# Optimization experiments

Measured on AMD Instinct MI355X. Metric: run time of the kernel, lower is better.

## Reference

```python
import jax, jax.numpy as jnp
import numpy as np

N = 50000        # nodes
E = 800000       # edges (avg degree 16)
C_IN = 64        # input_channels
H = 64           # hidden_channels
SLOPE = 0.01     # F.leaky_relu default negative_slope


def setup_inputs() -> dict:
    key = jax.random.key(0)
    ks = jax.random.split(key, 12)
    inp = {}
    inp["x"] = jax.random.normal(ks[0], (N, C_IN), dtype=jnp.float32)
    inp["edge_index"] = jax.random.randint(ks[1], (2, E), 0, N, dtype=jnp.int32)
    # SAGEConv params: lin_l (neighbors, with bias), lin_r (root, no bias)
    dims = [(C_IN, H), (H, H), (H, H)]
    for i, (ci, co) in enumerate(dims, start=1):
        s = 1.0 / np.sqrt(ci)
        inp[f"W_l{i}"] = jax.random.uniform(ks[2 * i], (ci, co), jnp.float32, -s, s)
        inp[f"b_l{i}"] = jnp.zeros((co,), jnp.float32)
        inp[f"W_r{i}"] = jax.random.uniform(ks[2 * i + 1], (ci, co), jnp.float32, -s, s)
    s = 1.0 / np.sqrt(H)
    inp["W_out"] = jax.random.uniform(ks[8], (H, 1), jnp.float32, -s, s)
    inp["b_out"] = jnp.zeros((1,), jnp.float32)
    return inp


def reference(x, edge_index, W_l1, b_l1, W_r1, W_l2, b_l2, W_r2,
              W_l3, b_l3, W_r3, W_out, b_out):
    src, dst = edge_index[0], edge_index[1]
    # per-destination degree for mean aggregation (isolated nodes -> 0)
    deg = jax.ops.segment_sum(jnp.ones((src.shape[0],), x.dtype), dst,
                              num_segments=N)
    inv_deg = (1.0 / jnp.maximum(deg, 1.0))[:, None]  # [N,1]

    def sage(h, Wl, bl, Wr):
        # gather source features, mean-reduce onto destinations
        mean_nb = jax.ops.segment_sum(h[src], dst, num_segments=N) * inv_deg
        out = mean_nb @ Wl + bl + h @ Wr
        # dropout is identity in eval mode
        return jax.nn.leaky_relu(out, SLOPE)

    h = sage(x, W_l1, b_l1, W_r1)
    h = sage(h, W_l2, b_l2, W_r2)
    h = sage(h, W_l3, b_l3, W_r3)
    return (h @ W_out + b_out).squeeze()  # [N]
```

## Files before the change

### kernel.cpp

```cpp
#include <hip/hip_runtime.h>

#define HD 64
#define SLOPE 0.01f
#define BSH 6
#define BNODES 64
#define CHUNK 4096
#define SLOT 1536


__global__ __launch_bounds__(256) void part_kernel(const int* __restrict__ ei,
                                                   int* __restrict__ bcur,
                                                   int* __restrict__ ebuf,
                                                   int E, int nb) {
    __shared__ int pk_s[CHUNK];
    __shared__ int mt_s[CHUNK];
    __shared__ int hist[784];
    __shared__ int sbase[784];
    const int t = threadIdx.x;
    const int c0 = blockIdx.x * CHUNK;
    const int cnt = min(CHUNK, E - c0);
    for (int i = t; i < nb; i += 256) hist[i] = 0;
    __syncthreads();
    for (int i = t; i < cnt; i += 256) {
        int src = ei[c0 + i];
        int dst = ei[E + c0 + i];
        int b = dst >> BSH;
        pk_s[i] = (src << BSH) | (dst & (BNODES - 1));
        int r = atomicAdd(&hist[b], 1);
        mt_s[i] = (b << 12) | r;
    }
    __syncthreads();
    for (int b = t; b < nb; b += 256) {
        int h = hist[b];
        if (h) sbase[b] = b * SLOT + atomicAdd(&bcur[b], h);
    }
    __syncthreads();
    for (int i = t; i < cnt; i += 256) {
        int m = mt_s[i];
        int b = m >> 12;
        ebuf[sbase[b] + (m & (CHUNK - 1))] = pk_s[i];
    }
}

__global__ __launch_bounds__(256) void bsort_kernel(const int* __restrict__ ebuf,
                                                    const int* __restrict__ bcnt,
                                                    int* __restrict__ colidx,
                                                    int* __restrict__ rowptr,
                                                    int* __restrict__ rowend,
                                                    float* __restrict__ invdeg,
                                                    int n) {
    __shared__ int cnt[BNODES];
    const int b = blockIdx.x;
    const int t = threadIdx.x;
    const int ebeg = b * SLOT;
    const int eend = ebeg + bcnt[b];
    if (t < BNODES) cnt[t] = 0;
    __syncthreads();
    for (int k = ebeg + t; k < eend; k += 256)
        atomicAdd(&cnt[ebuf[k] & (BNODES - 1)], 1);
    __syncthreads();
    if (t < BNODES) {
        int v = cnt[t];
        int x = v;
        #pragma unroll
        for (int d = 1; d < 64; d <<= 1) { int y = __shfl_up(x, d, 64); if (t >= d) x += y; }
        int excl = x - v;
        int node = b * BNODES + t;
        if (node < n) {
            rowptr[node] = ebeg + excl;
            rowend[node] = ebeg + excl + v;
            invdeg[node] = 1.0f / (float)((v > 1) ? v : 1);
        }
        cnt[t] = excl;
    }
    __syncthreads();
    for (int k = ebeg + t; k < eend; k += 256) {
        int p = ebuf[k];
        int r = atomicAdd(&cnt[p & (BNODES - 1)], 1);
        colidx[ebeg + r] = p >> BSH;
    }
}


__global__ __launch_bounds__(256) void tohalf_kernel(const float* __restrict__ in,
                                                     _Float16* __restrict__ out,
                                                     int n64) {
    int i = (blockIdx.x * 256 + threadIdx.x) * 8;
    if (i >= n64) return;
    float4 a = *(const float4*)(in + i);
    float4 b = *(const float4*)(in + i + 4);
    _Float16 o[8] = {(_Float16)a.x, (_Float16)a.y, (_Float16)a.z, (_Float16)a.w,
                     (_Float16)b.x, (_Float16)b.y, (_Float16)b.z, (_Float16)b.w};
    *(float4*)(out + i) = *(float4*)o;
}


#define FMA4(acc, am, b0, b1, b2, b3)                                  \
    acc.x += am.x * b0.x + am.y * b1.x + am.z * b2.x + am.w * b3.x;    \
    acc.y += am.x * b0.y + am.y * b1.y + am.z * b2.y + am.w * b3.y;    \
    acc.z += am.x * b0.z + am.y * b1.z + am.z * b2.z + am.w * b3.z;    \
    acc.w += am.x * b0.w + am.y * b1.w + am.z * b2.w + am.w * b3.w;

#define FUSED_BODY(EXTRA_SHARED)                                            \
    __shared__ float sA[64 * 68];            \
    __shared__ float sS[64 * 68];                            \
    EXTRA_SHARED                                                            \
    const int t = threadIdx.x;                                              \
    const int lane = t & 63;                                                \
    const int w = t >> 6;                                                   \
    const int base = blockIdx.x * 64;                                       \
    const int rows = min(64, n - base);                                     \
    const float4* __restrict__ hh4 = (const float4*)h_in;                   \
                                                       \
    _Pragma("unroll")                                                       \
    for (int idx = 0; idx < 4; ++idx) {                                     \
        int i = t + idx * 256;                                              \
        int r = i >> 4, cc = i & 15;                                        \
        float4 vs = {0.f, 0.f, 0.f, 0.f};                                   \
        if (r < rows) vs = hh4[(size_t)(base + r) * 16 + cc];               \
        *(float4*)(sS + r * 68 + 4 * cc) = vs;                              \
    }                                                                       \
                                  \
    {                                                                       \
        const int g = lane >> 3;                        \
        const int c8 = lane & 7;            \
        const float4* __restrict__ g4 = (const float4*)h16;                 \
        _Pragma("unroll")                                                   \
        for (int pass = 0; pass < 2; ++pass) {                              \
            const int r = w * 16 + pass * 8 + g;       \
            const int node = base + r;                                      \
            const bool valid = node < n;                                    \
            int beg = 0, end = 0; float idg = 0.f;                          \
            if (valid) {                                                    \
                beg = rowptr[node];                                         \
                end = rowend[node];                                         \
                idg = invdeg[node];                                         \
            }                                                               \
            const int deg = end - beg;                                      \
            int md = deg;                             \
            md = max(md, __shfl_xor(md, 8, 64));                            \
            md = max(md, __shfl_xor(md, 16, 64));                           \
            md = max(md, __shfl_xor(md, 32, 64));                           \
            float4 accA = {0.f, 0.f, 0.f, 0.f};                             \
            float4 accB = {0.f, 0.f, 0.f, 0.f};                             \
            for (int t0 = 0; t0 < md; t0 += 8) {                            \
                const int off = beg + t0 + c8;                              \
                int ci = (off < end) ? colidx[off] : 0;                     \
                int idx[8];                                                 \
                _Pragma("unroll")                                           \
                for (int k = 0; k < 8; ++k)                                 \
                    idx[k] = __shfl(ci, g * 8 + k, 64);                     \
                float4 vv[8];                                               \
                float sel[8];                                               \
                _Pragma("unroll")                                           \
                for (int k = 0; k < 8; ++k) {                               \
                    const bool p = (t0 + k) < deg;                          \
                    const int safe = p ? idx[k] : 0;                        \
                    sel[k] = p ? 1.0f : 0.0f;                               \
                    vv[k] = g4[(size_t)safe * 8 + c8];                      \
                }                                                           \
                _Pragma("unroll")                                           \
                for (int k = 0; k < 8; ++k) {                               \
                    const _Float16* hp = (const _Float16*)&vv[k];           \
                    accA.x += sel[k] * (float)hp[0];                        \
                    accA.y += sel[k] * (float)hp[1];                        \
                    accA.z += sel[k] * (float)hp[2];                        \
                    accA.w += sel[k] * (float)hp[3];                        \
                    accB.x += sel[k] * (float)hp[4];                        \
                    accB.y += sel[k] * (float)hp[5];                        \
                    accB.z += sel[k] * (float)hp[6];                        \
                    accB.w += sel[k] * (float)hp[7];                        \
                }                                                           \
            }                                                               \
            float4 oA = {accA.x * idg, accA.y * idg, accA.z * idg, accA.w * idg}; \
            float4 oB = {accB.x * idg, accB.y * idg, accB.z * idg, accB.w * idg}; \
            *(float4*)(sA + r * 68 + c8 * 8 + 0) = oA;                      \
            *(float4*)(sA + r * 68 + c8 * 8 + 4) = oB;                      \
        }                                                                   \
    }                                                                       \
    __syncthreads();                                                        \
      \
    const int r0 = t & 15;                                                  \
    const int jq = t >> 4;                                        \
    const int j0 = jq * 4;                                                  \
    const float4* __restrict__ Wl4 = (const float4*)Wl;                     \
    const float4* __restrict__ Wr4 = (const float4*)Wr;                     \
    const float4 bias = *(const float4*)(bl + j0);                          \
    float4 acc0 = bias, acc1 = bias, acc2 = bias, acc3 = bias;              \
    _Pragma("unroll 2")                                                     \
    for (int k4 = 0; k4 < 16; ++k4) {                                       \
        float4 b0 = Wl4[(4 * k4 + 0) * 16 + jq];                            \
        float4 b1 = Wl4[(4 * k4 + 1) * 16 + jq];                            \
        float4 b2 = Wl4[(4 * k4 + 2) * 16 + jq];                            \
        float4 b3 = Wl4[(4 * k4 + 3) * 16 + jq];                            \
        float4 a0 = *(const float4*)(sA + (r0 +  0) * 68 + 4 * k4);         \
        float4 a1 = *(const float4*)(sA + (r0 + 16) * 68 + 4 * k4);         \
        float4 a2 = *(const float4*)(sA + (r0 + 32) * 68 + 4 * k4);         \
        float4 a3 = *(const float4*)(sA + (r0 + 48) * 68 + 4 * k4);         \
        FMA4(acc0, a0, b0, b1, b2, b3)                                      \
        FMA4(acc1, a1, b0, b1, b2, b3)                                      \
        FMA4(acc2, a2, b0, b1, b2, b3)                                      \
        FMA4(acc3, a3, b0, b1, b2, b3)                                      \
        b0 = Wr4[(4 * k4 + 0) * 16 + jq];                                   \
        b1 = Wr4[(4 * k4 + 1) * 16 + jq];                                   \
        b2 = Wr4[(4 * k4 + 2) * 16 + jq];                                   \
        b3 = Wr4[(4 * k4 + 3) * 16 + jq];                                   \
        a0 = *(const float4*)(sS + (r0 +  0) * 68 + 4 * k4);                \
        a1 = *(const float4*)(sS + (r0 + 16) * 68 + 4 * k4);                \
        a2 = *(const float4*)(sS + (r0 + 32) * 68 + 4 * k4);                \
        a3 = *(const float4*)(sS + (r0 + 48) * 68 + 4 * k4);                \
        FMA4(acc0, a0, b0, b1, b2, b3)                                      \
        FMA4(acc1, a1, b0, b1, b2, b3)                                      \
        FMA4(acc2, a2, b0, b1, b2, b3)                                      \
        FMA4(acc3, a3, b0, b1, b2, b3)                                      \
    }                                                                       \
    acc0.x = (acc0.x > 0.f) ? acc0.x : SLOPE * acc0.x;                      \
    acc0.y = (acc0.y > 0.f) ? acc0.y : SLOPE * acc0.y;                      \
    acc0.z = (acc0.z > 0.f) ? acc0.z : SLOPE * acc0.z;                      \
    acc0.w = (acc0.w > 0.f) ? acc0.w : SLOPE * acc0.w;                      \
    acc1.x = (acc1.x > 0.f) ? acc1.x : SLOPE * acc1.x;                      \
    acc1.y = (acc1.y > 0.f) ? acc1.y : SLOPE * acc1.y;                      \
    acc1.z = (acc1.z > 0.f) ? acc1.z : SLOPE * acc1.z;                      \
    acc1.w = (acc1.w > 0.f) ? acc1.w : SLOPE * acc1.w;                      \
    acc2.x = (acc2.x > 0.f) ? acc2.x : SLOPE * acc2.x;                      \
    acc2.y = (acc2.y > 0.f) ? acc2.y : SLOPE * acc2.y;                      \
    acc2.z = (acc2.z > 0.f) ? acc2.z : SLOPE * acc2.z;                      \
    acc2.w = (acc2.w > 0.f) ? acc2.w : SLOPE * acc2.w;                      \
    acc3.x = (acc3.x > 0.f) ? acc3.x : SLOPE * acc3.x;                      \
    acc3.y = (acc3.y > 0.f) ? acc3.y : SLOPE * acc3.y;                      \
    acc3.z = (acc3.z > 0.f) ? acc3.z : SLOPE * acc3.z;                      \
    acc3.w = (acc3.w > 0.f) ? acc3.w : SLOPE * acc3.w;

__global__ __launch_bounds__(256, 4) void sage_fused(
    const _Float16* __restrict__ h16, const float* __restrict__ h_in,
    float* __restrict__ h_out, _Float16* __restrict__ h16_out,
    const int* __restrict__ rowptr, const int* __restrict__ rowend,
    const int* __restrict__ colidx, const float* __restrict__ invdeg,
    const float* __restrict__ Wl, const float* __restrict__ bl,
    const float* __restrict__ Wr, int n) {
    FUSED_BODY()
    #define STORE_ROW(S, ACC)                                               \
        { int r = r0 + 16 * S;                                              \
          if (r < rows) {                                                   \
              *(float4*)(h_out + (size_t)(base + r) * HD + j0) = ACC;       \
              _Float16 o[4] = {(_Float16)ACC.x, (_Float16)ACC.y,            \
                               (_Float16)ACC.z, (_Float16)ACC.w};           \
              *(float2*)(h16_out + (size_t)(base + r) * HD + j0)            \
                  = *(float2*)o;                                            \
          } }
    STORE_ROW(0, acc0)
    STORE_ROW(1, acc1)
    STORE_ROW(2, acc2)
    STORE_ROW(3, acc3)
    #undef STORE_ROW
}

__global__ __launch_bounds__(256, 4) void sage_fused_out(
    const _Float16* __restrict__ h16, const float* __restrict__ h_in,
    const int* __restrict__ rowptr, const int* __restrict__ rowend,
    const int* __restrict__ colidx, const float* __restrict__ invdeg,
    const float* __restrict__ Wl, const float* __restrict__ bl,
    const float* __restrict__ Wr,
    const float* __restrict__ Wout, const float* __restrict__ bout,
    float* __restrict__ out, int n) {
    FUSED_BODY(__shared__ float s_part[16][64];)
    const float4 w4 = *(const float4*)(Wout + j0);
    s_part[jq][r0 +  0] = acc0.x * w4.x + acc0.y * w4.y + acc0.z * w4.z + acc0.w * w4.w;
    s_part[jq][r0 + 16] = acc1.x * w4.x + acc1.y * w4.y + acc1.z * w4.z + acc1.w * w4.w;
    s_part[jq][r0 + 32] = acc2.x * w4.x + acc2.y * w4.y + acc2.z * w4.z + acc2.w * w4.w;
    s_part[jq][r0 + 48] = acc3.x * w4.x + acc3.y * w4.y + acc3.z * w4.z + acc3.w * w4.w;
    __syncthreads();
    if (t < 64) {
        float sum = 0.f;
        #pragma unroll
        for (int g2 = 0; g2 < 16; ++g2) sum += s_part[g2][t];
        if (t < rows) out[base + t] = sum + bout[0];
    }
}


extern "C" void kernel_launch(void* const* d_in, const int* in_sizes, int n_in,
                              void* d_out, int out_size, void* d_ws, size_t ws_size,
                              hipStream_t stream) {
    const float* x   = (const float*)d_in[0];
    const int* ei    = (const int*)d_in[1];
    const float* Wl1 = (const float*)d_in[2];
    const float* bl1 = (const float*)d_in[3];
    const float* Wr1 = (const float*)d_in[4];
    const float* Wl2 = (const float*)d_in[5];
    const float* bl2 = (const float*)d_in[6];
    const float* Wr2 = (const float*)d_in[7];
    const float* Wl3 = (const float*)d_in[8];
    const float* bl3 = (const float*)d_in[9];
    const float* Wr3 = (const float*)d_in[10];
    const float* Wout = (const float*)d_in[11];
    const float* bout = (const float*)d_in[12];
    float* out = (float*)d_out;

    const int N = in_sizes[0] / HD;
    const int E = in_sizes[1] / 2;
    const int NB = (N + BNODES - 1) >> BSH;

    float* hA     = (float*)d_ws;
    float* hB     = hA + (size_t)N * HD;
    _Float16* h16a = (_Float16*)(hB + (size_t)N * HD);
    _Float16* h16b = h16a + (size_t)N * HD;
    int* ebuf     = (int*)(h16b + (size_t)N * HD);
    int* colidx   = ebuf + (size_t)NB * SLOT;
    int* rowptr   = colidx + (size_t)NB * SLOT;
    int* rowend   = rowptr + N;
    float* invdeg = (float*)(rowend + N);
    int* bcur     = (int*)(invdeg + N);

    hipMemsetAsync(bcur, 0, 784 * sizeof(int), stream);

    part_kernel<<<(E + CHUNK - 1) / CHUNK, 256, 0, stream>>>(ei, bcur, ebuf, E, NB);
    bsort_kernel<<<NB, 256, 0, stream>>>(ebuf, bcur, colidx, rowptr, rowend,
                                         invdeg, N);

    const int n64 = N * HD;
    tohalf_kernel<<<(n64 / 8 + 255) / 256, 256, 0, stream>>>(x, h16a, n64);

    const int ggrid = (N + 63) / 64;

    sage_fused<<<ggrid, 256, 0, stream>>>(h16a, x, hA, h16b,
                                          rowptr, rowend, colidx, invdeg,
                                          Wl1, bl1, Wr1, N);
    sage_fused<<<ggrid, 256, 0, stream>>>(h16b, hA, hB, h16a,
                                          rowptr, rowend, colidx, invdeg,
                                          Wl2, bl2, Wr2, N);
    sage_fused_out<<<ggrid, 256, 0, stream>>>(h16a, hB,
                                              rowptr, rowend, colidx, invdeg,
                                              Wl3, bl3, Wr3, Wout, bout, out, N);
}
```

Baseline: 217.1 us.

## Drop fp32 hidden-state copies and fold fp16 conversion into bsort kernel

Each layer now reads its root features from the fp16 copy, converting to fp32 in shared memory, and no longer writes a separate fp32 output buffer. This removes one fp32 write and one fp32 read of the full node-feature matrix per layer. The standalone x-to-fp16 conversion kernel is merged into the CSR bucket-sort kernel as a grid-stride loop, saving a launch. The root term now uses fp16-rounded activations, which reduces accuracy slightly.

After: 205.0 us. -5.6%, faster.

```diff
diff --git a/kernel.cpp b/kernel.cpp
--- a/kernel.cpp
+++ b/kernel.cpp
@@ -48,7 +48,9 @@
                                                     int* __restrict__ rowptr,
                                                     int* __restrict__ rowend,
                                                     float* __restrict__ invdeg,
-                                                    int n) {
+                                                    const float* __restrict__ x,
+                                                    _Float16* __restrict__ h16a,
+                                                    int n, int n64) {
     __shared__ int cnt[BNODES];
     const int b = blockIdx.x;
     const int t = threadIdx.x;
@@ -61,10 +63,10 @@
     __syncthreads();
     if (t < BNODES) {
         int v = cnt[t];
-        int x = v;
+        int x2 = v;
         #pragma unroll
-        for (int d = 1; d < 64; d <<= 1) { int y = __shfl_up(x, d, 64); if (t >= d) x += y; }
-        int excl = x - v;
+        for (int d = 1; d < 64; d <<= 1) { int y = __shfl_up(x2, d, 64); if (t >= d) x2 += y; }
+        int excl = x2 - v;
         int node = b * BNODES + t;
         if (node < n) {
             rowptr[node] = ebeg + excl;
@@ -79,19 +81,15 @@
         int r = atomicAdd(&cnt[p & (BNODES - 1)], 1);
         colidx[ebeg + r] = p >> BSH;
     }
-}
-
-
-__global__ __launch_bounds__(256) void tohalf_kernel(const float* __restrict__ in,
-                                                     _Float16* __restrict__ out,
-                                                     int n64) {
-    int i = (blockIdx.x * 256 + threadIdx.x) * 8;
-    if (i >= n64) return;
-    float4 a = *(const float4*)(in + i);
-    float4 b = *(const float4*)(in + i + 4);
-    _Float16 o[8] = {(_Float16)a.x, (_Float16)a.y, (_Float16)a.z, (_Float16)a.w,
-                     (_Float16)b.x, (_Float16)b.y, (_Float16)b.z, (_Float16)b.w};
-    *(float4*)(out + i) = *(float4*)o;
+    const int total8 = n64 >> 3;
+    for (int i = b * 256 + t; i < total8; i += gridDim.x * 256) {
+        int e = i * 8;
+        float4 a = *(const float4*)(x + e);
+        float4 c = *(const float4*)(x + e + 4);
+        _Float16 o[8] = {(_Float16)a.x, (_Float16)a.y, (_Float16)a.z, (_Float16)a.w,
+                         (_Float16)c.x, (_Float16)c.y, (_Float16)c.z, (_Float16)c.w};
+        *(float4*)(h16a + e) = *(float4*)o;
+    }
 }
 
 
@@ -103,28 +101,31 @@
 
 #define FUSED_BODY(EXTRA_SHARED)                                            \
     __shared__ float sA[64 * 68];            \
-    __shared__ float sS[64 * 68];                            \
+    __shared__ float sS[64 * 68];                       \
     EXTRA_SHARED                                                            \
     const int t = threadIdx.x;                                              \
     const int lane = t & 63;                                                \
     const int w = t >> 6;                                                   \
     const int base = blockIdx.x * 64;                                       \
     const int rows = min(64, n - base);                                     \
-    const float4* __restrict__ hh4 = (const float4*)h_in;                   \
-                                                       \
+    const float4* __restrict__ g4 = (const float4*)h16_in;                  \
+        \
     _Pragma("unroll")                                                       \
-    for (int idx = 0; idx < 4; ++idx) {                                     \
-        int i = t + idx * 256;                                              \
-        int r = i >> 4, cc = i & 15;                                        \
-        float4 vs = {0.f, 0.f, 0.f, 0.f};                                   \
-        if (r < rows) vs = hh4[(size_t)(base + r) * 16 + cc];               \
-        *(float4*)(sS + r * 68 + 4 * cc) = vs;                              \
+    for (int idx = 0; idx < 2; ++idx) {                                     \
+        int i = t + idx * 256;                                  \
+        int r = i >> 3, cc = i & 7;                                         \
+        float4 raw = {0.f, 0.f, 0.f, 0.f};                                  \
+        if (r < rows) raw = g4[(size_t)(base + r) * 8 + cc];                \
+        const _Float16* hp = (const _Float16*)&raw;                         \
+        float4 lo = {(float)hp[0], (float)hp[1], (float)hp[2], (float)hp[3]}; \
+        float4 hi = {(float)hp[4], (float)hp[5], (float)hp[6], (float)hp[7]}; \
+        *(float4*)(sS + r * 68 + cc * 8 + 0) = lo;                          \
+        *(float4*)(sS + r * 68 + cc * 8 + 4) = hi;                          \
     }                                                                       \
                                   \
     {                                                                       \
         const int g = lane >> 3;                        \
         const int c8 = lane & 7;            \
-        const float4* __restrict__ g4 = (const float4*)h16;                 \
         _Pragma("unroll")                                                   \
         for (int pass = 0; pass < 2; ++pass) {                              \
             const int r = w * 16 + pass * 8 + g;       \
@@ -232,8 +233,7 @@
     acc3.w = (acc3.w > 0.f) ? acc3.w : SLOPE * acc3.w;
 
 __global__ __launch_bounds__(256, 4) void sage_fused(
-    const _Float16* __restrict__ h16, const float* __restrict__ h_in,
-    float* __restrict__ h_out, _Float16* __restrict__ h16_out,
+    const _Float16* __restrict__ h16_in, _Float16* __restrict__ h16_out,
     const int* __restrict__ rowptr, const int* __restrict__ rowend,
     const int* __restrict__ colidx, const float* __restrict__ invdeg,
     const float* __restrict__ Wl, const float* __restrict__ bl,
@@ -242,7 +242,6 @@
     #define STORE_ROW(S, ACC)                                               \
         { int r = r0 + 16 * S;                                              \
           if (r < rows) {                                                   \
-              *(float4*)(h_out + (size_t)(base + r) * HD + j0) = ACC;       \
               _Float16 o[4] = {(_Float16)ACC.x, (_Float16)ACC.y,            \
                                (_Float16)ACC.z, (_Float16)ACC.w};           \
               *(float2*)(h16_out + (size_t)(base + r) * HD + j0)            \
@@ -256,7 +255,7 @@
 }
 
 __global__ __launch_bounds__(256, 4) void sage_fused_out(
-    const _Float16* __restrict__ h16, const float* __restrict__ h_in,
+    const _Float16* __restrict__ h16_in,
     const int* __restrict__ rowptr, const int* __restrict__ rowend,
     const int* __restrict__ colidx, const float* __restrict__ invdeg,
     const float* __restrict__ Wl, const float* __restrict__ bl,
@@ -300,10 +299,9 @@
     const int N = in_sizes[0] / HD;
     const int E = in_sizes[1] / 2;
     const int NB = (N + BNODES - 1) >> BSH;
-
-    float* hA     = (float*)d_ws;
-    float* hB     = hA + (size_t)N * HD;
-    _Float16* h16a = (_Float16*)(hB + (size_t)N * HD);
+    const int n64 = N * HD;
+
+    _Float16* h16a = (_Float16*)d_ws;
     _Float16* h16b = h16a + (size_t)N * HD;
     int* ebuf     = (int*)(h16b + (size_t)N * HD);
     int* colidx   = ebuf + (size_t)NB * SLOT;
@@ -316,20 +314,17 @@
 
     part_kernel<<<(E + CHUNK - 1) / CHUNK, 256, 0, stream>>>(ei, bcur, ebuf, E, NB);
     bsort_kernel<<<NB, 256, 0, stream>>>(ebuf, bcur, colidx, rowptr, rowend,
-                                         invdeg, N);
-
-    const int n64 = N * HD;
-    tohalf_kernel<<<(n64 / 8 + 255) / 256, 256, 0, stream>>>(x, h16a, n64);
+                                         invdeg, x, h16a, N, n64);
 
     const int ggrid = (N + 63) / 64;
 
-    sage_fused<<<ggrid, 256, 0, stream>>>(h16a, x, hA, h16b,
+    sage_fused<<<ggrid, 256, 0, stream>>>(h16a, h16b,
                                           rowptr, rowend, colidx, invdeg,
                                           Wl1, bl1, Wr1, N);
-    sage_fused<<<ggrid, 256, 0, stream>>>(h16b, hA, hB, h16a,
+    sage_fused<<<ggrid, 256, 0, stream>>>(h16b, h16a,
                                           rowptr, rowend, colidx, invdeg,
                                           Wl2, bl2, Wr2, N);
-    sage_fused_out<<<ggrid, 256, 0, stream>>>(h16a, hB,
+    sage_fused_out<<<ggrid, 256, 0, stream>>>(h16a,
                                               rowptr, rowend, colidx, invdeg,
                                               Wl3, bl3, Wr3, Wout, bout, out, N);
 }
```
